# Performance work log

Measured on AMD Instinct MI355X. Metric: run time of the kernel, lower is better.

The kernel has to match this reference:

```python
import jax, jax.numpy as jnp
import numpy as np

N_QUBITS = 12
N_LAYERS = 3
N_CHUNKS = 12
CHUNK = 4
BATCH = 2048


def _u3(theta, phi, lam):
    # PennyLane U3 = [[cos(t/2), -e^{i l} sin(t/2)], [e^{i p} sin(t/2), e^{i(p+l)} cos(t/2)]]
    ct = jnp.cos(theta / 2).astype(jnp.complex64)
    st = jnp.sin(theta / 2).astype(jnp.complex64)
    ep = jnp.exp(1j * phi.astype(jnp.complex64))
    el = jnp.exp(1j * lam.astype(jnp.complex64))
    return jnp.stack([jnp.stack([ct, -el * st]), jnp.stack([ep * st, ep * el * ct])])


def _apply_1q(state, U, w):
    # state: (2,)*N_QUBITS
    s = jnp.moveaxis(state, w, 0)
    s = jnp.tensordot(U, s, axes=1)
    return jnp.moveaxis(s, 0, w)


def _apply_cnot(state, c, t):
    s = jnp.moveaxis(state, (c, t), (0, 1))
    s = jnp.stack([s[0], jnp.flip(s[1], axis=0)], axis=0)
    return jnp.moveaxis(s, (0, 1), (c, t))


def _circuit(params):
    # params: [N_CHUNKS, 3] -> expval PauliZ per wire, shape [N_QUBITS]
    state = jnp.zeros((2,) * N_QUBITS, jnp.complex64).at[(0,) * N_QUBITS].set(1.0)
    for _ in range(N_LAYERS):
        for i in range(N_CHUNKS):
            state = _apply_1q(state, _u3(params[i, 0], params[i, 1], params[i, 2]), i)
        for i in range(N_QUBITS):
            state = _apply_cnot(state, i, (i + 1) % N_QUBITS)
    p = jnp.abs(state) ** 2
    sign = jnp.array([1.0, -1.0], p.dtype)
    zs = []
    for i in range(N_QUBITS):
        marg = p.sum(axis=tuple(a for a in range(N_QUBITS) if a != i))
        zs.append(jnp.dot(marg, sign))
    return jnp.stack(zs)


def setup_inputs() -> dict:
    key = jax.random.key(0)
    ks = jax.random.split(key, 7)
    return {
        "x": jax.random.normal(ks[0], (BATCH, 48), jnp.float32),
        "reupload_weights": jax.random.normal(ks[1], (N_CHUNKS, 3, CHUNK), jnp.float32) * 0.1,
        "reupload_bias": jax.random.normal(ks[2], (N_CHUNKS, 3), jnp.float32) * 0.1,
        "w1": jax.random.normal(ks[3], (64, N_QUBITS), jnp.float32) * 0.1,
        "b1": jax.random.normal(ks[4], (64,), jnp.float32) * 0.1,
        "w2": jax.random.normal(ks[5], (256, 64), jnp.float32) * 0.1,
        "b2": jax.random.normal(ks[6], (256,), jnp.float32) * 0.1,
    }


def reference(x, reupload_weights, reupload_bias, w1, b1, w2, b2):
    chunks = x.reshape(-1, N_CHUNKS, CHUNK)  # [B, 12, 4]
    # per-chunk affine map: [12,3,4] @ [B,12,4] -> [B,12,3]
    params = jnp.einsum("cpk,bck->bcp", reupload_weights, chunks) + reupload_bias
    qz = jax.vmap(_circuit)(params)  # [B, 12]
    h = jax.nn.relu(qz @ w1.T + b1)
    return h @ w2.T + b2
```

## Files before the change

### kernel.cpp

```cpp
#include <hip/hip_runtime.h>
#include <hip/hip_fp16.h>
#include <math.h>

typedef _Float16 half8 __attribute__((ext_vector_type(8)));
typedef float f32x4 __attribute__((ext_vector_type(4)));

__device__ __forceinline__ int pfx4(int x) {
    return (x ^ (x << 1) ^ (x << 2) ^ (x << 3)) & 15;
}

__global__ __attribute__((amdgpu_flat_work_group_size(256, 256), amdgpu_waves_per_eu(4, 4)))
void qreup_kernel(const float* __restrict__ x, const float* __restrict__ rw,
                  const float* __restrict__ rb,
                  const float* __restrict__ w1, const float* __restrict__ b1,
                  const float* __restrict__ w2, const float* __restrict__ b2,
                  float* __restrict__ out)
{
    __shared__ __align__(16) char lds[32768];
    char* const wl = lds;

    const int t = threadIdx.x;
    const int b = blockIdx.x;
    const int l15 = t & 15, q = (t >> 4) & 3, wv = t >> 6;

    float* const uL = (float*)(lds + 16384);
    if (t < 12) {
        const float4 xv = ((const float4*)x)[b * 12 + t];
        float prm[3];
        #pragma unroll
        for (int p = 0; p < 3; ++p) {
            const float4 wvv = ((const float4*)rw)[t * 3 + p];
            prm[p] = rb[t * 3 + p] + wvv.x * xv.x + wvv.y * xv.y + wvv.z * xv.z + wvv.w * xv.w;
        }
        float st_, ct_; sincosf(0.5f * prm[0], &st_, &ct_);
        float sp_, cp_; sincosf(prm[1], &sp_, &cp_);
        float sl_, cl_; sincosf(prm[2], &sl_, &cl_);
        const float cpl = cp_ * cl_ - sp_ * sl_;
        const float spl = sp_ * cl_ + cp_ * sl_;
        ((float4*)uL)[t * 2]     = make_float4(ct_, 0.0f, -cl_ * st_, -sl_ * st_);
        ((float4*)uL)[t * 2 + 1] = make_float4(cp_ * st_, sp_ * st_, cpl * ct_, spl * ct_);
    }
    __syncthreads();

    {
        const int mp = t >> 4, mm = t & 15;
        #pragma unroll
        for (int g = 0; g < 3; ++g) {
            const float* p0 = uL + g * 32 + ((mp & 1) * 4 + (mm & 1) * 2);
            float wr = p0[0], wi = p0[1];
            #pragma unroll
            for (int bq = 1; bq < 4; ++bq) {
                const float* p = uL + g * 32 + bq * 8 + ((mp >> bq) & 1) * 4 + ((mm >> bq) & 1) * 2;
                const float br = p[0], bi = p[1];
                const float nr = wr * br - wi * bi, ni = wr * bi + wi * br;
                wr = nr; wi = ni;
            }
            const _Float16 hr = (_Float16)wr, hi_ = (_Float16)wi;
            const _Float16 lr = (_Float16)(wr - (float)hr), li = (_Float16)(wi - (float)hi_);
            union { _Float16 h[2]; unsigned int u; } ph, pl_;
            ph.h[0] = hr;  ph.h[1] = hi_;
            pl_.h[0] = lr; pl_.h[1] = li;
            *(unsigned int*)(wl + g * 2048 +        mp * 64 + mm * 4) = ph.u;
            *(unsigned int*)(wl + g * 2048 + 1024 + mp * 64 + mm * 4) = pl_.u;
        }
    }
    __syncthreads();

    half8 ArH[3], ArL[3], AiH[3], AiL[3];
    #pragma unroll
    for (int g = 0; g < 3; ++g) {
        #pragma unroll
        for (int hl = 0; hl < 2; ++hl) {
            int4 raw = *(const int4*)(wl + g * 2048 + hl * 1024 + l15 * 64 + q * 16);
            int re4[4], im4[4];
            int rr[4] = {raw.x, raw.y, raw.z, raw.w};
            #pragma unroll
            for (int i = 0; i < 4; ++i) {
                re4[i] = rr[i] ^ 0x80000000;
                im4[i] = (int)(((unsigned)rr[i] >> 16) | ((unsigned)rr[i] << 16));
            }
            half8 hre, him;
            __builtin_memcpy(&hre, re4, 16);
            __builtin_memcpy(&him, im4, 16);
            if (hl == 0) { ArH[g] = hre; AiH[g] = him; }
            else         { ArL[g] = hre; AiL[g] = him; }
        }
    }

    const int Ml = pfx4(l15);
    const int piL = (Ml >> 3) & 1;

    float A0 = 0.f, AT0 = 0.f, AT01 = 0.f, AR0 = 0.f, AR01 = 0.f;
    char* rbuf = lds;
    char* wbuf = lds + 16384;

    #pragma unroll 1
    for (int L = 0; L < 3; ++L) {
        if (L) __syncthreads();
        #pragma unroll
        for (int T = 0; T < 4; ++T) {
            const int tt = wv * 4 + T;
            half8 bfr;
            if (L == 0) {
                half8 z = {};
                if (t == 0 && T == 0) z[0] = (_Float16)1.0f;
                bfr = z;
            } else {
                const int nu = 16 * tt + l15;
                const int al = ((l15 >> 1) & 1) | ((((l15 >> 1) ^ (l15 >> 2)) & 1) << 1);
                const int be = ((tt >> 1) ^ (tt >> 2)) & 1;
                int4 raw = *(const int4*)(rbuf + 64 * (nu ^ be) + 16 * (q ^ al));
                if (tt & 8) {
                    int tmp = raw.x; raw.x = raw.y; raw.y = tmp;
                    tmp = raw.z; raw.z = raw.w; raw.w = tmp;
                }
                __builtin_memcpy(&bfr, &raw, 16);
            }
            f32x4 cre = {0.f,0.f,0.f,0.f}, cim = {0.f,0.f,0.f,0.f};
            cre = __builtin_amdgcn_mfma_f32_16x16x32_f16(ArH[0], bfr, cre, 0, 0, 0);
            cre = __builtin_amdgcn_mfma_f32_16x16x32_f16(ArL[0], bfr, cre, 0, 0, 0);
            cim = __builtin_amdgcn_mfma_f32_16x16x32_f16(AiH[0], bfr, cim, 0, 0, 0);
            cim = __builtin_amdgcn_mfma_f32_16x16x32_f16(AiL[0], bfr, cim, 0, 0, 0);
            const int als = q ^ ((tt >> 1) & 3);
            const int bes = (tt ^ q) & 1;
            const int D = 4 * (l15 ^ (als << 2));
            unsigned p4[4];
            #pragma unroll
            for (int r = 0; r < 4; ++r) {
                __half2 hp = __floats2half2_rn(cre[r], cim[r]);
                p4[r] = *(unsigned int*)&hp;
            }
            char* rowb = wbuf + 64 * (4 * q + 16 * tt) + D;
            const unsigned s0 = bes ? p4[1] : p4[0];
            const unsigned s1 = bes ? p4[0] : p4[1];
            const unsigned s2 = bes ? p4[3] : p4[2];
            const unsigned s3 = bes ? p4[2] : p4[3];
            *(unsigned int*)(rowb      ) = s0;
            *(unsigned int*)(rowb +  64) = s1;
            *(unsigned int*)(rowb + 128) = s2;
            *(unsigned int*)(rowb + 192) = s3;
        }
        { char* tmp = rbuf; rbuf = wbuf; wbuf = tmp; }

        __syncthreads();
        #pragma unroll
        for (int Tp = 0; Tp < 2; ++Tp) {
            unsigned pe[4], po[4];
            #pragma unroll
            for (int hf = 0; hf < 2; ++hf) {
                const int T = Tp * 2 + hf;
                const int tt = wv * 4 + T;
                const int nu = tt + 16 * l15;
                const int al = ((tt >> 2) & 3) ^ ((l15 >> 1) & 3);
                const int be = (l15 ^ (tt >> 2)) & 1;
                int4 raw = *(const int4*)(rbuf + 64 * (nu ^ be) + 16 * (q ^ al));
                half8 bfr; __builtin_memcpy(&bfr, &raw, 16);
                f32x4 cre = {0.f,0.f,0.f,0.f}, cim = {0.f,0.f,0.f,0.f};
                cre = __builtin_amdgcn_mfma_f32_16x16x32_f16(ArH[1], bfr, cre, 0, 0, 0);
                cre = __builtin_amdgcn_mfma_f32_16x16x32_f16(ArL[1], bfr, cre, 0, 0, 0);
                cim = __builtin_amdgcn_mfma_f32_16x16x32_f16(AiH[1], bfr, cim, 0, 0, 0);
                cim = __builtin_amdgcn_mfma_f32_16x16x32_f16(AiL[1], bfr, cim, 0, 0, 0);
                #pragma unroll
                for (int r = 0; r < 4; ++r) {
                    __half2 hp = __floats2half2_rn(cre[r], cim[r]);
                    if (hf == 0) pe[r] = *(unsigned int*)&hp;
                    else         po[r] = *(unsigned int*)&hp;
                }
            }
            const int tt0 = wv * 4 + Tp * 2;
            const int als = ((tt0 >> 1) & 3) ^ q;
            const int bes = q & 1;
            const int D = 4 * (l15 ^ (als << 2));
            #pragma unroll
            for (int r = 0; r < 4; ++r) {
                char* base = wbuf + 64 * (tt0 + 16 * (4 * q + r)) + D;
                const unsigned lo = bes ? po[r] : pe[r];
                const unsigned hi = bes ? pe[r] : po[r];
                *(unsigned int*)(base     ) = lo;
                *(unsigned int*)(base + 64) = hi;
            }
        }
        { char* tmp = rbuf; rbuf = wbuf; wbuf = tmp; }

        __syncthreads();
        #pragma unroll
        for (int T = 0; T < 4; ++T) {
            const int tt = wv * 4 + T;
            const int nu = l15 + 16 * tt;
            const int al = ((l15 >> 1) & 3) ^ ((tt >> 2) & 3);
            const int be = (tt >> 2) & 1;
            int4 raw = *(const int4*)(rbuf + 64 * (nu ^ be) + 16 * (q ^ al));
            half8 bfr; __builtin_memcpy(&bfr, &raw, 16);
            f32x4 cre = {0.f,0.f,0.f,0.f}, cim = {0.f,0.f,0.f,0.f};
            cre = __builtin_amdgcn_mfma_f32_16x16x32_f16(ArH[2], bfr, cre, 0, 0, 0);
            cre = __builtin_amdgcn_mfma_f32_16x16x32_f16(ArL[2], bfr, cre, 0, 0, 0);
            cim = __builtin_amdgcn_mfma_f32_16x16x32_f16(AiH[2], bfr, cim, 0, 0, 0);
            cim = __builtin_amdgcn_mfma_f32_16x16x32_f16(AiL[2], bfr, cim, 0, 0, 0);
            if (L < 2) {
                const int taub = pfx4(tt);
                const int lowH = (piL ? 15 : 0) ^ taub;
                const int s    = (lowH >> 3) & 1;
                const int als  = ((lowH >> 1) & 1) | ((((lowH >> 1) ^ (lowH >> 2)) & 1) << 1);
                const int bes  = q & 1;
                const int D = 4 * (Ml ^ (als << 2));
                #pragma unroll
                for (int r = 0; r < 4; ++r) {
                    const int rho = pfx4(4 * q + r);
                    const int H = lowH | (((s ? 15 : 0) ^ rho) << 4);
                    __half2 hp = __floats2half2_rn(cre[r], cim[r]);
                    *(unsigned int*)(wbuf + 64 * (H ^ bes) + D) = *(unsigned int*)&hp;
                }
            } else {
                const int sT0 = T & 1, sT01 = (T ^ (T >> 1)) & 1;
                #pragma unroll
                for (int r = 0; r < 4; ++r) {
                    const float pr = cre[r] * cre[r] + cim[r] * cim[r];
                    A0 += pr;
                    AT0  += sT0 ? -pr : pr;
                    AT01 += sT01 ? -pr : pr;
                    AR0  += (sT01 ^ (r & 1)) ? -pr : pr;
                    AR01 += (sT01 ^ ((r ^ (r >> 1)) & 1)) ? -pr : pr;
                }
            }
        }
        { char* tmp = rbuf; rbuf = wbuf; wbuf = tmp; }
    }

    const int pl = __popc(l15) & 1;
    const int wv0 = wv & 1, wv1 = (wv >> 1) & 1, wv01 = wv0 ^ wv1;
    const int q0 = q & 1, q1 = (q >> 1) & 1;
    float zp[12];
    zp[1] = (__popc(l15 & 3) & 1) ? -A0 : A0;
    zp[2] = (__popc(l15 & 7) & 1) ? -A0 : A0;
    zp[3] = pl ? -A0 : A0;
    zp[4] = pl ? -AT0 : AT0;
    zp[5] = pl ? -AT01 : AT01;
    zp[6] = (pl ^ wv0) ? -AT01 : AT01;
    zp[7] = (pl ^ wv0 ^ wv1) ? -AT01 : AT01;
    zp[8] = (pl ^ wv01) ? -AR0 : AR0;
    zp[9] = (pl ^ wv01) ? -AR01 : AR01;
    zp[10] = (pl ^ wv01 ^ q0) ? -AR01 : AR01;
    zp[11] = (pl ^ wv01 ^ q0 ^ q1) ? -AR01 : AR01;
    zp[0]  = ((l15 & 1) ^ pl ^ wv01 ^ q0 ^ q1) ? -AR01 : AR01;

    #pragma unroll
    for (int i = 0; i < 12; ++i) {
        float vv = zp[i];
        #pragma unroll
        for (int off = 32; off > 0; off >>= 1)
            vv += __shfl_xor(vv, off, 64);
        zp[i] = vv;
    }

    __syncthreads();
    float* stf  = (float*)lds;
    float* zred = stf;
    float* qzs  = stf + 48;
    float* hbuf = stf + 64;

    if ((t & 63) == 0) {
        #pragma unroll
        for (int i = 0; i < 12; ++i) zred[wv * 12 + i] = zp[i];
    }
    __syncthreads();
    if (t < 12)
        qzs[t] = zred[t] + zred[12 + t] + zred[24 + t] + zred[36 + t];
    __syncthreads();

    if (t < 64) {
        float acc = b1[t];
        #pragma unroll
        for (int i = 0; i < 12; ++i) acc += qzs[i] * w1[t * 12 + i];
        hbuf[t] = fmaxf(acc, 0.0f);
    }
    __syncthreads();
    float acc = b2[t];
    #pragma unroll 4
    for (int k4 = 0; k4 < 16; ++k4) {
        const float4 wvv = ((const float4*)w2)[t * 16 + k4];
        acc += wvv.x * hbuf[k4 * 4 + 0] + wvv.y * hbuf[k4 * 4 + 1]
             + wvv.z * hbuf[k4 * 4 + 2] + wvv.w * hbuf[k4 * 4 + 3];
    }
    out[b * 256 + t] = acc;
}

extern "C" void kernel_launch(void* const* d_in, const int* in_sizes, int n_in,
                              void* d_out, int out_size, void* d_ws, size_t ws_size,
                              hipStream_t stream) {
    const float* x  = (const float*)d_in[0];
    const float* rw = (const float*)d_in[1];
    const float* rb = (const float*)d_in[2];
    const float* w1 = (const float*)d_in[3];
    const float* b1 = (const float*)d_in[4];
    const float* w2 = (const float*)d_in[5];
    const float* b2 = (const float*)d_in[6];
    float* out = (float*)d_out;
    (void)d_ws; (void)ws_size;

    const int batch = in_sizes[0] / 48;
    qreup_kernel<<<batch, 256, 0, stream>>>(x, rw, rb, w1, b1, w2, b2, out);
}
```

Before: 96.81 us.

## Pair MFMA tiles for wider LDS stores and butterfly-share signed Z reductions

In the first two layers the final gate stage now processes tiles in pairs (T and 3-T), packs both half2 results and writes them together with simpler address math, replacing per-element address computation. The end-of-circuit PauliZ reduction is rewritten as a shared butterfly of signed shuffles, so the twelve expectation values reuse intermediate sums instead of each doing six full shuffles. Wave-level signs are applied when storing to LDS. This cuts shuffle count and address arithmetic but relies on carefully derived sign patterns.

```diff
diff --git a/kernel.cpp b/kernel.cpp
--- a/kernel.cpp
+++ b/kernel.cpp
@@ -8,6 +8,8 @@
 __device__ __forceinline__ int pfx4(int x) {
     return (x ^ (x << 1) ^ (x << 2) ^ (x << 3)) & 15;
 }
+
+__device__ __forceinline__ float shx(float v, int m) { return __shfl_xor(v, m, 64); }
 
 __global__ __attribute__((amdgpu_flat_work_group_size(256, 256), amdgpu_waves_per_eu(4, 4)))
 void qreup_kernel(const float* __restrict__ x, const float* __restrict__ rw,
@@ -183,74 +185,113 @@
         { char* tmp = rbuf; rbuf = wbuf; wbuf = tmp; }
 
         __syncthreads();
-        #pragma unroll
-        for (int T = 0; T < 4; ++T) {
-            const int tt = wv * 4 + T;
-            const int nu = l15 + 16 * tt;
-            const int al = ((l15 >> 1) & 3) ^ ((tt >> 2) & 3);
-            const int be = (tt >> 2) & 1;
-            int4 raw = *(const int4*)(rbuf + 64 * (nu ^ be) + 16 * (q ^ al));
-            half8 bfr; __builtin_memcpy(&bfr, &raw, 16);
-            f32x4 cre = {0.f,0.f,0.f,0.f}, cim = {0.f,0.f,0.f,0.f};
-            cre = __builtin_amdgcn_mfma_f32_16x16x32_f16(ArH[2], bfr, cre, 0, 0, 0);
-            cre = __builtin_amdgcn_mfma_f32_16x16x32_f16(ArL[2], bfr, cre, 0, 0, 0);
-            cim = __builtin_amdgcn_mfma_f32_16x16x32_f16(AiH[2], bfr, cim, 0, 0, 0);
-            cim = __builtin_amdgcn_mfma_f32_16x16x32_f16(AiL[2], bfr, cim, 0, 0, 0);
-            if (L < 2) {
-                const int taub = pfx4(tt);
-                const int lowH = (piL ? 15 : 0) ^ taub;
-                const int s    = (lowH >> 3) & 1;
-                const int als  = ((lowH >> 1) & 1) | ((((lowH >> 1) ^ (lowH >> 2)) & 1) << 1);
+        if (L < 2) {
+            #pragma unroll
+            for (int pr = 0; pr < 2; ++pr) {
+                const int Ta = pr, Tb = 3 - pr;
+                unsigned va[4], vb[4];
+                #pragma unroll
+                for (int hf = 0; hf < 2; ++hf) {
+                    const int T = hf ? Tb : Ta;
+                    const int tt = wv * 4 + T;
+                    const int nu = l15 + 16 * tt;
+                    const int al = ((l15 >> 1) & 3) ^ ((tt >> 2) & 3);
+                    const int be = (tt >> 2) & 1;
+                    int4 raw = *(const int4*)(rbuf + 64 * (nu ^ be) + 16 * (q ^ al));
+                    half8 bfr; __builtin_memcpy(&bfr, &raw, 16);
+                    f32x4 cre = {0.f,0.f,0.f,0.f}, cim = {0.f,0.f,0.f,0.f};
+                    cre = __builtin_amdgcn_mfma_f32_16x16x32_f16(ArH[2], bfr, cre, 0, 0, 0);
+                    cre = __builtin_amdgcn_mfma_f32_16x16x32_f16(ArL[2], bfr, cre, 0, 0, 0);
+                    cim = __builtin_amdgcn_mfma_f32_16x16x32_f16(AiH[2], bfr, cim, 0, 0, 0);
+                    cim = __builtin_amdgcn_mfma_f32_16x16x32_f16(AiL[2], bfr, cim, 0, 0, 0);
+                    #pragma unroll
+                    for (int r = 0; r < 4; ++r) {
+                        __half2 hp = __floats2half2_rn(cre[r], cim[r]);
+                        if (hf == 0) va[r] = *(unsigned int*)&hp;
+                        else         vb[r] = *(unsigned int*)&hp;
+                    }
+                }
+                const int tta  = wv * 4 + Ta;
+                const int lowHa = (piL ? 15 : 0) ^ pfx4(tta);
+                const int s    = (lowHa >> 3) & 1;
+                const int als  = ((lowHa >> 1) & 1) | ((((lowHa >> 1) ^ (lowHa >> 2)) & 1) << 1);
                 const int bes  = q & 1;
                 const int D = 4 * (Ml ^ (als << 2));
+                const int cb = (lowHa ^ bes) & 1;
+                char* base = wbuf + 64 * ((lowHa ^ bes) & ~1) + D;
                 #pragma unroll
                 for (int r = 0; r < 4; ++r) {
-                    const int rho = pfx4(4 * q + r);
-                    const int H = lowH | (((s ? 15 : 0) ^ rho) << 4);
-                    __half2 hp = __floats2half2_rn(cre[r], cim[r]);
-                    *(unsigned int*)(wbuf + 64 * (H ^ bes) + D) = *(unsigned int*)&hp;
-                }
-            } else {
+                    const int hiN = (s ? 15 : 0) ^ pfx4(4 * q + r);
+                    const unsigned lo = cb ? vb[r] : va[r];
+                    const unsigned hi = cb ? va[r] : vb[r];
+                    *(unsigned int*)(base + 1024 * hiN     ) = lo;
+                    *(unsigned int*)(base + 1024 * hiN + 64) = hi;
+                }
+            }
+        } else {
+            #pragma unroll
+            for (int T = 0; T < 4; ++T) {
+                const int tt = wv * 4 + T;
+                const int nu = l15 + 16 * tt;
+                const int al = ((l15 >> 1) & 3) ^ ((tt >> 2) & 3);
+                const int be = (tt >> 2) & 1;
+                int4 raw = *(const int4*)(rbuf + 64 * (nu ^ be) + 16 * (q ^ al));
+                half8 bfr; __builtin_memcpy(&bfr, &raw, 16);
+                f32x4 cre = {0.f,0.f,0.f,0.f}, cim = {0.f,0.f,0.f,0.f};
+                cre = __builtin_amdgcn_mfma_f32_16x16x32_f16(ArH[2], bfr, cre, 0, 0, 0);
+                cre = __builtin_amdgcn_mfma_f32_16x16x32_f16(ArL[2], bfr, cre, 0, 0, 0);
+                cim = __builtin_amdgcn_mfma_f32_16x16x32_f16(AiH[2], bfr, cim, 0, 0, 0);
+                cim = __builtin_amdgcn_mfma_f32_16x16x32_f16(AiL[2], bfr, cim, 0, 0, 0);
                 const int sT0 = T & 1, sT01 = (T ^ (T >> 1)) & 1;
                 #pragma unroll
                 for (int r = 0; r < 4; ++r) {
-                    const float pr = cre[r] * cre[r] + cim[r] * cim[r];
-                    A0 += pr;
-                    AT0  += sT0 ? -pr : pr;
-                    AT01 += sT01 ? -pr : pr;
-                    AR0  += (sT01 ^ (r & 1)) ? -pr : pr;
-                    AR01 += (sT01 ^ ((r ^ (r >> 1)) & 1)) ? -pr : pr;
+                    const float pr2 = cre[r] * cre[r] + cim[r] * cim[r];
+                    A0 += pr2;
+                    AT0  += sT0 ? -pr2 : pr2;
+                    AT01 += sT01 ? -pr2 : pr2;
+                    AR0  += (sT01 ^ (r & 1)) ? -pr2 : pr2;
+                    AR01 += (sT01 ^ ((r ^ (r >> 1)) & 1)) ? -pr2 : pr2;
                 }
             }
         }
         { char* tmp = rbuf; rbuf = wbuf; wbuf = tmp; }
     }
 
-    const int pl = __popc(l15) & 1;
     const int wv0 = wv & 1, wv1 = (wv >> 1) & 1, wv01 = wv0 ^ wv1;
-    const int q0 = q & 1, q1 = (q >> 1) & 1;
-    float zp[12];
-    zp[1] = (__popc(l15 & 3) & 1) ? -A0 : A0;
-    zp[2] = (__popc(l15 & 7) & 1) ? -A0 : A0;
-    zp[3] = pl ? -A0 : A0;
-    zp[4] = pl ? -AT0 : AT0;
-    zp[5] = pl ? -AT01 : AT01;
-    zp[6] = (pl ^ wv0) ? -AT01 : AT01;
-    zp[7] = (pl ^ wv0 ^ wv1) ? -AT01 : AT01;
-    zp[8] = (pl ^ wv01) ? -AR0 : AR0;
-    zp[9] = (pl ^ wv01) ? -AR01 : AR01;
-    zp[10] = (pl ^ wv01 ^ q0) ? -AR01 : AR01;
-    zp[11] = (pl ^ wv01 ^ q0 ^ q1) ? -AR01 : AR01;
-    zp[0]  = ((l15 & 1) ^ pl ^ wv01 ^ q0 ^ q1) ? -AR01 : AR01;
-
-    #pragma unroll
-    for (int i = 0; i < 12; ++i) {
-        float vv = zp[i];
-        #pragma unroll
-        for (int off = 32; off > 0; off >>= 1)
-            vv += __shfl_xor(vv, off, 64);
-        zp[i] = vv;
-    }
+    float v, tw;
+    v = A0;
+    v -= shx(v, 1);
+    v -= shx(v, 2);
+    tw = shx(v, 4);
+    float a3 = v + tw, a7f = v - tw;
+    tw = shx(a3, 8);  float S1 = a3 + tw;
+    tw = shx(a7f, 8); float S2 = a7f + tw;
+    float S3 = a7f - tw;
+    S1 += shx(S1, 16); S1 += shx(S1, 32);
+    S2 += shx(S2, 16); S2 += shx(S2, 32);
+    S3 += shx(S3, 16); S3 += shx(S3, 32);
+    float S4 = AT0, S5 = AT01, S8 = AR0;
+    S4 -= shx(S4, 1); S4 -= shx(S4, 2); S4 -= shx(S4, 4); S4 -= shx(S4, 8);
+    S4 += shx(S4, 16); S4 += shx(S4, 32);
+    S5 -= shx(S5, 1); S5 -= shx(S5, 2); S5 -= shx(S5, 4); S5 -= shx(S5, 8);
+    S5 += shx(S5, 16); S5 += shx(S5, 32);
+    S8 -= shx(S8, 1); S8 -= shx(S8, 2); S8 -= shx(S8, 4); S8 -= shx(S8, 8);
+    S8 += shx(S8, 16); S8 += shx(S8, 32);
+    v = AR01;
+    v -= shx(v, 2); v -= shx(v, 4); v -= shx(v, 8);
+    tw = shx(v, 1);
+    float U = v - tw;
+    float W = v + tw;
+    tw = shx(U, 16);
+    float P = U + tw;
+    float Q = U - tw;
+    tw = shx(W, 16);
+    float R = W - tw;
+    float S9 = P + shx(P, 32);
+    tw = shx(Q, 32);
+    float S10 = Q + tw;
+    float S11 = Q - tw;
+    float S0 = R - shx(R, 32);
 
     __syncthreads();
     float* stf  = (float*)lds;
@@ -259,8 +300,19 @@
     float* hbuf = stf + 64;
 
     if ((t & 63) == 0) {
-        #pragma unroll
-        for (int i = 0; i < 12; ++i) zred[wv * 12 + i] = zp[i];
+        float* zr = zred + wv * 12;
+        zr[0]  = wv01 ? -S0  : S0;
+        zr[1]  = S1;
+        zr[2]  = S2;
+        zr[3]  = S3;
+        zr[4]  = S4;
+        zr[5]  = S5;
+        zr[6]  = wv0 ? -S5 : S5;
+        zr[7]  = (wv0 ^ wv1) ? -S5 : S5;
+        zr[8]  = wv01 ? -S8  : S8;
+        zr[9]  = wv01 ? -S9  : S9;
+        zr[10] = wv01 ? -S10 : S10;
+        zr[11] = wv01 ? -S11 : S11;
     }
     __syncthreads();
     if (t < 12)
```

New measurement: 93.58 us. 3.3% less time.
